# Performance work log

Measured on AMD Instinct MI355X. Metric: run time of the kernel, lower is better.

The kernel has to match this reference:

```python
import jax, jax.numpy as jnp
import numpy as np

C_M, C_Z, C = 256, 128, 32
N_SEQ, N_RES = 128, 256


def setup_inputs() -> dict:
    key = jax.random.key(0)
    ks = jax.random.split(key, 9)
    s = 0.02
    return {
        "m": jax.random.normal(ks[0], (N_SEQ, N_RES, C_M), dtype=jnp.float32),
        "ln_w": jnp.ones((C_M,), dtype=jnp.float32),
        "ln_b": jnp.zeros((C_M,), dtype=jnp.float32),
        "w1": jax.random.normal(ks[1], (C, C_M), dtype=jnp.float32) * s,
        "b1": jnp.zeros((C,), dtype=jnp.float32),
        "w2": jax.random.normal(ks[2], (C, C_M), dtype=jnp.float32) * s,
        "b2": jnp.zeros((C,), dtype=jnp.float32),
        "wo": jax.random.normal(ks[3], (C_Z, C * C), dtype=jnp.float32) * s,
        "bo": jnp.zeros((C_Z,), dtype=jnp.float32),
    }


def reference(m, ln_w, ln_b, w1, b1, w2, b2, wo, bo):
    n_seq = m.shape[-3]
    # LayerNorm over c_m
    mu = jnp.mean(m, axis=-1, keepdims=True)
    var = jnp.mean(jnp.square(m - mu), axis=-1, keepdims=True)
    mn = (m - mu) * jax.lax.rsqrt(var + 1e-5) * ln_w + ln_b
    # dual projections to c channels: [s, i, c]
    a = jnp.einsum('sim,cm->sic', mn, w1) + b1
    b = jnp.einsum('sjm,dm->sjd', mn, w2) + b2
    # outer product mean contracted over sequence axis: [i, j, c, d]
    o = jnp.einsum('sic,sjd->ijcd', a, b)
    o = o.reshape(o.shape[0], o.shape[1], C * C)
    # output projection and mean over sequences
    z = (jnp.einsum('ijk,zk->ijz', o, wo) + bo) / n_seq
    return z
```

## Files before the change

kernel.cpp:

```cpp
#include <hip/hip_runtime.h>
#include <hip/hip_bf16.h>
#include <stdint.h>

#define N_RES 256
#define CMDIM 256

typedef __attribute__((ext_vector_type(8))) short bf16x8;
typedef __attribute__((ext_vector_type(4))) float f32x4;
typedef __attribute__((ext_vector_type(2))) unsigned int u32x2;

__device__ __forceinline__ unsigned short f32_to_bf16(float f) {
    union { float f; unsigned int u; } v; v.f = f;
    unsigned int u = v.u;
    return (unsigned short)((u + 0x7FFFu + ((u >> 16) & 1u)) >> 16);
}


__global__ __launch_bounds__(256) void k_prep(
    const float* __restrict__ w1, const float* __restrict__ w2,
    const float* __restrict__ wo,
    unsigned short* __restrict__ Wbf, unsigned short* __restrict__ wof)
{
    int t = blockIdx.x * 256 + threadIdx.x;
    if (t < 16384) {
        int ch = t >> 8, cm = t & 255;
        float v = (ch < 32) ? w1[ch * 256 + cm] : w2[(ch - 32) * 256 + cm];
        int addr = ((ch >> 4) * 8 + (cm >> 5)) * 512 + ((cm >> 3) & 3) * 128 + (ch & 15) * 8 + (cm & 7);
        Wbf[addr] = f32_to_bf16(v);
    }
    if (t < 131072) {
        int zo = t >> 10, k = t & 1023;
        int addr = ((zo >> 4) * 32 + (k >> 5)) * 512 + ((k >> 3) & 3) * 128 + (zo & 15) * 8 + (k & 7);
        wof[addr] = f32_to_bf16(wo[t]);
    }
}

__global__ __launch_bounds__(256) void k_ln_proj(
    const float* __restrict__ m, const float* __restrict__ lnw, const float* __restrict__ lnb,
    const float* __restrict__ b1, const float* __restrict__ b2,
    const unsigned short* __restrict__ Wbf,
    unsigned short* __restrict__ A2f, unsigned short* __restrict__ B2f)
{
    __shared__ unsigned short mn[32 * 256];
    int b = blockIdx.x;
    int i = b >> 2, sblk = b & 3;
    int tid = threadIdx.x;
    int wv = tid >> 6, lane = tid & 63;
    int quad = lane >> 4, l15 = lane & 15;

    f32x4 lw = *(const f32x4*)(lnw + lane * 4);
    f32x4 lb = *(const f32x4*)(lnb + lane * 4);

    #pragma unroll
    for (int r = 0; r < 8; ++r) {
        int sl = wv * 8 + r;
        int s = sblk * 32 + sl;
        const float* row = m + ((size_t)s * N_RES + i) * CMDIM;
        f32x4 x = *(const f32x4*)(row + lane * 4);
        float s1 = x[0] + x[1] + x[2] + x[3];
        float s2 = x[0]*x[0] + x[1]*x[1] + x[2]*x[2] + x[3]*x[3];
        #pragma unroll
        for (int off = 32; off; off >>= 1) {
            s1 += __shfl_xor(s1, off);
            s2 += __shfl_xor(s2, off);
        }
        float mu = s1 * (1.0f / 256.0f);
        float var = s2 * (1.0f / 256.0f) - mu * mu;
        float rstd = rsqrtf(var + 1e-5f);
        float n0 = (x[0] - mu) * rstd * lw[0] + lb[0];
        float n1 = (x[1] - mu) * rstd * lw[1] + lb[1];
        float n2 = (x[2] - mu) * rstd * lw[2] + lb[2];
        float n3 = (x[3] - mu) * rstd * lw[3] + lb[3];
        unsigned int p0 = (unsigned)f32_to_bf16(n0) | ((unsigned)f32_to_bf16(n1) << 16);
        unsigned int p1 = (unsigned)f32_to_bf16(n2) | ((unsigned)f32_to_bf16(n3) << 16);
        int chunk = lane >> 1;
        int pos = (chunk & 16) | ((chunk ^ sl) & 15);
        unsigned int* dst = (unsigned int*)((char*)mn + sl * 512 + pos * 16 + (lane & 1) * 8);
        dst[0] = p0; dst[1] = p1;
    }
    __syncthreads();

    bf16x8 af[8];
    #pragma unroll
    for (int ks = 0; ks < 8; ++ks)
        af[ks] = *(const bf16x8*)(Wbf + (wv * 8 + ks) * 512 + lane * 8);

    f32x4 acc[2];
    acc[0] = (f32x4){0.f, 0.f, 0.f, 0.f};
    acc[1] = (f32x4){0.f, 0.f, 0.f, 0.f};
    #pragma unroll
    for (int ks = 0; ks < 8; ++ks) {
        #pragma unroll
        for (int nb = 0; nb < 2; ++nb) {
            int sl = nb * 16 + l15;
            int chunk = ks * 4 + quad;
            int pos = (chunk & 16) | ((chunk ^ sl) & 15);
            bf16x8 bf = *(const bf16x8*)((char*)mn + sl * 512 + pos * 16);
            acc[nb] = __builtin_amdgcn_mfma_f32_16x16x32_bf16(af[ks], bf, acc[nb], 0, 0, 0);
        }
    }

    const float* bsrc = (wv < 2) ? b1 : b2;
    f32x4 bias = *(const f32x4*)(bsrc + (wv & 1) * 16 + quad * 4);
    unsigned short* dst = (wv < 2) ? A2f : B2f;
    #pragma unroll
    for (int nb = 0; nb < 2; ++nb) {
        int s = sblk * 32 + nb * 16 + l15;
        int shi = ((s >> 3) & 3) * 128 + (s & 7);
        #pragma unroll
        for (int reg = 0; reg < 4; ++reg) {
            int ic = i * 32 + (wv & 1) * 16 + quad * 4 + reg;
            int addr = ((ic >> 4) * 4 + sblk) * 512 + shi + (ic & 15) * 8;
            dst[addr] = f32_to_bf16(acc[nb][reg] + bias[reg]);
        }
    }
}

__global__ __launch_bounds__(256, 2) void k_fused(
    const unsigned short* __restrict__ A2f, const unsigned short* __restrict__ B2f,
    const unsigned short* __restrict__ wof, const float* __restrict__ bo,
    float* __restrict__ out)
{
    __shared__ char olds[32 * 2048];
    int bx = blockIdx.x;
    int by = blockIdx.y;
    int tid = threadIdx.x, wv = tid >> 6, lane = tid & 63;
    int quad = lane >> 4, l15 = lane & 15;
    int wm = wv & 1, wn = wv >> 1;

    bf16x8 bn[4][4];
    #pragma unroll
    for (int ks = 0; ks < 4; ++ks)
        #pragma unroll
        for (int nb = 0; nb < 4; ++nb)
            bn[ks][nb] = *(const bf16x8*)(A2f + (size_t)(((bx * 8 + wn * 4 + nb) * 4 + ks) * 512) + lane * 8);

    for (int pass = 0; pass < 2; ++pass) {
        f32x4 acc[4][4];
        #pragma unroll
        for (int a = 0; a < 4; ++a)
            #pragma unroll
            for (int b = 0; b < 4; ++b) acc[a][b] = (f32x4){0.f, 0.f, 0.f, 0.f};

        #pragma unroll
        for (int ks = 0; ks < 4; ++ks) {
            bf16x8 am[4];
            #pragma unroll
            for (int mb = 0; mb < 4; ++mb)
                am[mb] = *(const bf16x8*)(B2f + (size_t)(((by * 16 + pass * 8 + wm * 4 + mb) * 4 + ks) * 512) + lane * 8);
            #pragma unroll
            for (int mb = 0; mb < 4; ++mb)
                #pragma unroll
                for (int nb = 0; nb < 4; ++nb)
                    acc[mb][nb] = __builtin_amdgcn_mfma_f32_16x16x32_bf16(am[mb], bn[ks][nb], acc[mb][nb], 0, 0, 0);
        }

        #pragma unroll
        for (int mb = 0; mb < 4; ++mb) {
            int m_ = wm * 64 + mb * 16 + quad * 4;
            int d0 = m_ & 31;
            int jl = pass * 4 + (m_ >> 5);
            #pragma unroll
            for (int nb = 0; nb < 4; ++nb) {
                int n_ = wn * 64 + nb * 16 + l15;
                int c = n_ & 31, il = n_ >> 5;
                int pair = il * 8 + jl;
                int e0 = c * 32 + d0;
                f32x4 a4 = acc[mb][nb];
                unsigned int p0 = (unsigned)f32_to_bf16(a4[0]) | ((unsigned)f32_to_bf16(a4[1]) << 16);
                unsigned int p1 = (unsigned)f32_to_bf16(a4[2]) | ((unsigned)f32_to_bf16(a4[3]) << 16);
                u32x2 pv = {p0, p1};
                int chunk = e0 >> 3;
                int phys = chunk ^ ((chunk >> 3) & 7) ^ (pair & 7);
                *(u32x2*)(olds + pair * 2048 + phys * 16 + (e0 & 7) * 2) = pv;
            }
        }
    }
    __syncthreads();

    f32x4 acc2[2][2];
    #pragma unroll
    for (int a = 0; a < 2; ++a)
        #pragma unroll
        for (int b = 0; b < 2; ++b) acc2[a][b] = (f32x4){0.f, 0.f, 0.f, 0.f};

    const unsigned short* wbase = wof + (size_t)(wv * 2 * 32) * 512 + lane * 8;

    bf16x8 afA[2], bfA[2], afB[2], bfB[2];
    #pragma unroll
    for (int zb = 0; zb < 2; ++zb)
        afA[zb] = *(const bf16x8*)(wbase + (size_t)(zb * 32) * 512);
    #pragma unroll
    for (int pb = 0; pb < 2; ++pb) {
        int pair = pb * 16 + l15;
        int chunk = quad;
        int phys = chunk ^ ((chunk >> 3) & 7) ^ (pair & 7);
        bfA[pb] = *(const bf16x8*)(olds + pair * 2048 + phys * 16);
    }

    #pragma unroll 2
    for (int kt = 0; kt < 32; kt += 2) {
        #pragma unroll
        for (int zb = 0; zb < 2; ++zb)
            afB[zb] = *(const bf16x8*)(wbase + (size_t)(zb * 32 + kt + 1) * 512);
        #pragma unroll
        for (int pb = 0; pb < 2; ++pb) {
            int pair = pb * 16 + l15;
            int chunk = (kt + 1) * 4 + quad;
            int phys = chunk ^ ((chunk >> 3) & 7) ^ (pair & 7);
            bfB[pb] = *(const bf16x8*)(olds + pair * 2048 + phys * 16);
        }
        #pragma unroll
        for (int zb = 0; zb < 2; ++zb)
            #pragma unroll
            for (int pb = 0; pb < 2; ++pb)
                acc2[zb][pb] = __builtin_amdgcn_mfma_f32_16x16x32_bf16(afA[zb], bfA[pb], acc2[zb][pb], 0, 0, 0);
        if (kt + 2 < 32) {
            #pragma unroll
            for (int zb = 0; zb < 2; ++zb)
                afA[zb] = *(const bf16x8*)(wbase + (size_t)(zb * 32 + kt + 2) * 512);
            #pragma unroll
            for (int pb = 0; pb < 2; ++pb) {
                int pair = pb * 16 + l15;
                int chunk = (kt + 2) * 4 + quad;
                int phys = chunk ^ ((chunk >> 3) & 7) ^ (pair & 7);
                bfA[pb] = *(const bf16x8*)(olds + pair * 2048 + phys * 16);
            }
        }
        #pragma unroll
        for (int zb = 0; zb < 2; ++zb)
            #pragma unroll
            for (int pb = 0; pb < 2; ++pb)
                acc2[zb][pb] = __builtin_amdgcn_mfma_f32_16x16x32_bf16(afB[zb], bfB[pb], acc2[zb][pb], 0, 0, 0);
    }

    #pragma unroll
    for (int zb = 0; zb < 2; ++zb) {
        int zo = wv * 32 + zb * 16 + quad * 4;
        f32x4 b4 = *(const f32x4*)(bo + zo);
        #pragma unroll
        for (int pb = 0; pb < 2; ++pb) {
            int pair = pb * 16 + l15;
            int i = bx * 4 + (pair >> 3);
            int j = by * 8 + (pair & 7);
            f32x4 v;
            #pragma unroll
            for (int reg = 0; reg < 4; ++reg)
                v[reg] = (acc2[zb][pb][reg] + b4[reg]) * (1.0f / 128.0f);
            *(f32x4*)(out + ((size_t)(i * 256 + j)) * 128 + zo) = v;
        }
    }
}

extern "C" void kernel_launch(void* const* d_in, const int* in_sizes, int n_in,
                              void* d_out, int out_size, void* d_ws, size_t ws_size,
                              hipStream_t stream) {
    const float* m   = (const float*)d_in[0];
    const float* lnw = (const float*)d_in[1];
    const float* lnb = (const float*)d_in[2];
    const float* w1  = (const float*)d_in[3];
    const float* b1  = (const float*)d_in[4];
    const float* w2  = (const float*)d_in[5];
    const float* b2  = (const float*)d_in[6];
    const float* wo  = (const float*)d_in[7];
    const float* bo  = (const float*)d_in[8];
    float* out = (float*)d_out;
    char* ws = (char*)d_ws;

    unsigned short* Wbf = (unsigned short*)(ws);
    unsigned short* wof = (unsigned short*)(ws + 32768);
    unsigned short* A2f = (unsigned short*)(ws + 32768 + 262144);
    unsigned short* B2f = (unsigned short*)(ws + 32768 + 262144 + 2097152);

    hipLaunchKernelGGL(k_prep, dim3(512), dim3(256), 0, stream, w1, w2, wo, Wbf, wof);
    hipLaunchKernelGGL(k_ln_proj, dim3(1024), dim3(256), 0, stream,
                       m, lnw, lnb, b1, b2, Wbf, A2f, B2f);
    hipLaunchKernelGGL(k_fused, dim3(64, 32), dim3(256), 0, stream,
                       A2f, B2f, wof, bo, out);
}
```

Before: 147.6 us.

## Stage projection stores via LDS, prefetch B operands, re-swizzle olds, deepen pipeline

The LN-projection kernel now writes its outputs to a shared-memory staging buffer and then issues one coalesced 16-byte global store per thread, replacing scattered 2-byte stores. In the fused kernel, the B2f operand is double-buffered across k-steps and the pass loop is fully unrolled. The shared outer-product tile is laid out chunk-major with an XOR swizzle on pair index. The output-projection loop now prefetches three k-steps ahead instead of one. These changes target store inefficiency, global-load latency and LDS bank conflicts, at the cost of more registers, which could reduce occupancy under the 2-block launch bound.

```diff
diff --git a/kernel.cpp b/kernel.cpp
--- a/kernel.cpp
+++ b/kernel.cpp
@@ -42,6 +42,7 @@
     unsigned short* __restrict__ A2f, unsigned short* __restrict__ B2f)
 {
     __shared__ unsigned short mn[32 * 256];
+    __shared__ unsigned short stg[2048];
     int b = blockIdx.x;
     int i = b >> 2, sblk = b & 3;
     int tid = threadIdx.x;
@@ -102,18 +103,20 @@
 
     const float* bsrc = (wv < 2) ? b1 : b2;
     f32x4 bias = *(const f32x4*)(bsrc + (wv & 1) * 16 + quad * 4);
-    unsigned short* dst = (wv < 2) ? A2f : B2f;
+    unsigned short* sbase = stg + (wv >> 1) * 1024 + (wv & 1) * 512 + quad * 32;
     #pragma unroll
     for (int nb = 0; nb < 2; ++nb) {
-        int s = sblk * 32 + nb * 16 + l15;
-        int shi = ((s >> 3) & 3) * 128 + (s & 7);
-        #pragma unroll
-        for (int reg = 0; reg < 4; ++reg) {
-            int ic = i * 32 + (wv & 1) * 16 + quad * 4 + reg;
-            int addr = ((ic >> 4) * 4 + sblk) * 512 + shi + (ic & 15) * 8;
-            dst[addr] = f32_to_bf16(acc[nb][reg] + bias[reg]);
-        }
-    }
+        int sl = nb * 16 + l15;
+        int soff = ((sl >> 3) & 3) * 128 + (sl & 7);
+        #pragma unroll
+        for (int reg = 0; reg < 4; ++reg)
+            sbase[soff + reg * 8] = f32_to_bf16(acc[nb][reg] + bias[reg]);
+    }
+    __syncthreads();
+
+    int part = tid >> 7, blk = (tid >> 6) & 1, l = tid & 63;
+    unsigned short* gdst = (part ? B2f : A2f) + ((i * 2 + blk) * 4 + sblk) * 512 + l * 8;
+    *(bf16x8*)gdst = *(const bf16x8*)(stg + tid * 8);
 }
 
 __global__ __launch_bounds__(256, 2) void k_fused(
@@ -121,7 +124,7 @@
     const unsigned short* __restrict__ wof, const float* __restrict__ bo,
     float* __restrict__ out)
 {
-    __shared__ char olds[32 * 2048];
+    __shared__ char olds[65536];
     int bx = blockIdx.x;
     int by = blockIdx.y;
     int tid = threadIdx.x, wv = tid >> 6, lane = tid & 63;
@@ -135,6 +138,7 @@
         for (int nb = 0; nb < 4; ++nb)
             bn[ks][nb] = *(const bf16x8*)(A2f + (size_t)(((bx * 8 + wn * 4 + nb) * 4 + ks) * 512) + lane * 8);
 
+    #pragma unroll
     for (int pass = 0; pass < 2; ++pass) {
         f32x4 acc[4][4];
         #pragma unroll
@@ -142,17 +146,25 @@
             #pragma unroll
             for (int b = 0; b < 4; ++b) acc[a][b] = (f32x4){0.f, 0.f, 0.f, 0.f};
 
+        bf16x8 amC[4], amN[4];
+        #pragma unroll
+        for (int mb = 0; mb < 4; ++mb)
+            amC[mb] = *(const bf16x8*)(B2f + (size_t)(((by * 16 + pass * 8 + wm * 4 + mb) * 4 + 0) * 512) + lane * 8);
+
         #pragma unroll
         for (int ks = 0; ks < 4; ++ks) {
-            bf16x8 am[4];
-            #pragma unroll
-            for (int mb = 0; mb < 4; ++mb)
-                am[mb] = *(const bf16x8*)(B2f + (size_t)(((by * 16 + pass * 8 + wm * 4 + mb) * 4 + ks) * 512) + lane * 8);
+            if (ks < 3) {
+                #pragma unroll
+                for (int mb = 0; mb < 4; ++mb)
+                    amN[mb] = *(const bf16x8*)(B2f + (size_t)(((by * 16 + pass * 8 + wm * 4 + mb) * 4 + ks + 1) * 512) + lane * 8);
+            }
             #pragma unroll
             for (int mb = 0; mb < 4; ++mb)
                 #pragma unroll
                 for (int nb = 0; nb < 4; ++nb)
-                    acc[mb][nb] = __builtin_amdgcn_mfma_f32_16x16x32_bf16(am[mb], bn[ks][nb], acc[mb][nb], 0, 0, 0);
+                    acc[mb][nb] = __builtin_amdgcn_mfma_f32_16x16x32_bf16(amC[mb], bn[ks][nb], acc[mb][nb], 0, 0, 0);
+            #pragma unroll
+            for (int mb = 0; mb < 4; ++mb) amC[mb] = amN[mb];
         }
 
         #pragma unroll
@@ -166,13 +178,13 @@
                 int c = n_ & 31, il = n_ >> 5;
                 int pair = il * 8 + jl;
                 int e0 = c * 32 + d0;
+                int chunk = e0 >> 3;
+                int phys = pair ^ (chunk & 31);
                 f32x4 a4 = acc[mb][nb];
                 unsigned int p0 = (unsigned)f32_to_bf16(a4[0]) | ((unsigned)f32_to_bf16(a4[1]) << 16);
                 unsigned int p1 = (unsigned)f32_to_bf16(a4[2]) | ((unsigned)f32_to_bf16(a4[3]) << 16);
                 u32x2 pv = {p0, p1};
-                int chunk = e0 >> 3;
-                int phys = chunk ^ ((chunk >> 3) & 7) ^ (pair & 7);
-                *(u32x2*)(olds + pair * 2048 + phys * 16 + (e0 & 7) * 2) = pv;
+                *(u32x2*)(olds + chunk * 512 + phys * 16 + (e0 & 7) * 2) = pv;
             }
         }
     }
@@ -186,52 +198,42 @@
 
     const unsigned short* wbase = wof + (size_t)(wv * 2 * 32) * 512 + lane * 8;
 
-    bf16x8 afA[2], bfA[2], afB[2], bfB[2];
-    #pragma unroll
-    for (int zb = 0; zb < 2; ++zb)
-        afA[zb] = *(const bf16x8*)(wbase + (size_t)(zb * 32) * 512);
-    #pragma unroll
-    for (int pb = 0; pb < 2; ++pb) {
-        int pair = pb * 16 + l15;
-        int chunk = quad;
-        int phys = chunk ^ ((chunk >> 3) & 7) ^ (pair & 7);
-        bfA[pb] = *(const bf16x8*)(olds + pair * 2048 + phys * 16);
-    }
-
-    #pragma unroll 2
-    for (int kt = 0; kt < 32; kt += 2) {
+    bf16x8 af[4][2], bfr[4][2];
+    #pragma unroll
+    for (int p = 0; p < 3; ++p) {
         #pragma unroll
         for (int zb = 0; zb < 2; ++zb)
-            afB[zb] = *(const bf16x8*)(wbase + (size_t)(zb * 32 + kt + 1) * 512);
+            af[p][zb] = *(const bf16x8*)(wbase + (size_t)(zb * 32 + p) * 512);
         #pragma unroll
         for (int pb = 0; pb < 2; ++pb) {
             int pair = pb * 16 + l15;
-            int chunk = (kt + 1) * 4 + quad;
-            int phys = chunk ^ ((chunk >> 3) & 7) ^ (pair & 7);
-            bfB[pb] = *(const bf16x8*)(olds + pair * 2048 + phys * 16);
-        }
-        #pragma unroll
-        for (int zb = 0; zb < 2; ++zb)
-            #pragma unroll
-            for (int pb = 0; pb < 2; ++pb)
-                acc2[zb][pb] = __builtin_amdgcn_mfma_f32_16x16x32_bf16(afA[zb], bfA[pb], acc2[zb][pb], 0, 0, 0);
-        if (kt + 2 < 32) {
+            int chunk = p * 4 + quad;
+            int phys = pair ^ (chunk & 31);
+            bfr[p][pb] = *(const bf16x8*)(olds + chunk * 512 + phys * 16);
+        }
+    }
+
+    #pragma unroll
+    for (int kt = 0; kt < 32; ++kt) {
+        int slot = kt & 3;
+        if (kt + 3 < 32) {
+            int pf = kt + 3, ps = pf & 3;
             #pragma unroll
             for (int zb = 0; zb < 2; ++zb)
-                afA[zb] = *(const bf16x8*)(wbase + (size_t)(zb * 32 + kt + 2) * 512);
+                af[ps][zb] = *(const bf16x8*)(wbase + (size_t)(zb * 32 + pf) * 512);
             #pragma unroll
             for (int pb = 0; pb < 2; ++pb) {
                 int pair = pb * 16 + l15;
-                int chunk = (kt + 2) * 4 + quad;
-                int phys = chunk ^ ((chunk >> 3) & 7) ^ (pair & 7);
-                bfA[pb] = *(const bf16x8*)(olds + pair * 2048 + phys * 16);
+                int chunk = pf * 4 + quad;
+                int phys = pair ^ (chunk & 31);
+                bfr[ps][pb] = *(const bf16x8*)(olds + chunk * 512 + phys * 16);
             }
         }
         #pragma unroll
         for (int zb = 0; zb < 2; ++zb)
             #pragma unroll
             for (int pb = 0; pb < 2; ++pb)
-                acc2[zb][pb] = __builtin_amdgcn_mfma_f32_16x16x32_bf16(afB[zb], bfB[pb], acc2[zb][pb], 0, 0, 0);
+                acc2[zb][pb] = __builtin_amdgcn_mfma_f32_16x16x32_bf16(af[slot][zb], bfr[slot][pb], acc2[zb][pb], 0, 0, 0);
     }
 
     #pragma unroll
```

Result: faster. 139.2 us (-5.6%).
